# Performance work log

Measured on AMD Instinct MI355X. Metric: run time of the kernel, lower is better.

The kernel has to match this reference:

```python
import jax, jax.numpy as jnp
import numpy as np

B, N, D, H, O = 20000, 32, 128, 256, 128
ATT_SLOPE = 0.01   # nn.LeakyReLU() default inside self.att
ALPHA = 0.2        # leakyrelu slope for attention scores


def _lrelu(v, slope):
    return jnp.where(v > 0, v, slope * v)


def setup_inputs() -> dict:
    key = jax.random.key(0)
    ks = jax.random.split(key, 6)
    x = jax.random.normal(ks[0], (B, D), dtype=jnp.float32)
    neibs = jax.random.normal(ks[1], (B * N, D), dtype=jnp.float32)
    # torch Linear weight is [out,in]; we store transposed [in,out] for x @ W
    W_att = jax.random.normal(ks[2], (D, H), dtype=jnp.float32) / np.sqrt(D)
    W_fcx = jax.random.normal(ks[3], (D, O), dtype=jnp.float32) / np.sqrt(D)
    W_fcn = jax.random.normal(ks[4], (D, O), dtype=jnp.float32) / np.sqrt(D)
    a = jax.random.normal(ks[5], (2 * H, 1), dtype=jnp.float32) * (1.414 * np.sqrt(6.0 / (2 * H + 1)))
    return {"x": x, "neibs": neibs, "W_att": W_att, "W_fcx": W_fcx, "W_fcn": W_fcn, "a": a}


def reference(x, neibs, W_att, W_fcx, W_fcn, a):
    b = x.shape[0]
    n = neibs.shape[0] // b
    # self.att = Linear(no bias) + LeakyReLU(default 0.01)
    x_att = _lrelu(x @ W_att, ATT_SLOPE)                       # [B,H]
    neib_att = _lrelu(neibs @ W_att, ATT_SLOPE).reshape(b, n, -1)  # [B,N,H]
    # cat([x_att.repeat, neib_att]) @ a  ==  x_att @ a[:H] + neib_att @ a[H:]
    h = W_att.shape[1]
    e = _lrelu(x_att @ a[:h, 0] + neib_att @ a[h:, 0][..., None] if False else
               (x_att @ a[:h, 0])[:, None] + jnp.einsum('bnh,h->bn', neib_att, a[h:, 0]), ALPHA)  # [B,N]
    attention = jax.nn.softmax(e, axis=1)                      # softmax over neighbors
    # dropout skipped (eval mode / training=False)
    agg_neib = jnp.einsum('bnd,bn->bd', neibs.reshape(b, n, -1), attention)  # [B,D]
    out = jnp.concatenate([x @ W_fcx, agg_neib @ W_fcn], axis=1)  # combine_fn = cat dim=1
    out = jax.nn.relu(out)                                     # activation
    return out
```

## Files before the change

kernel.cpp:

```cpp
#include <hip/hip_runtime.h>
#include <hip/hip_bf16.h>


#define BB 20000
#define NN 32
#define DD 128
#define HH 256
#define OO 128
#define MB 4
#define ROWS 144
#define XR0 128
#define AG0 132

typedef __bf16 bf16x8 __attribute__((ext_vector_type(8)));
typedef __bf16 bf16x4 __attribute__((ext_vector_type(4)));
typedef float f32x4 __attribute__((ext_vector_type(4)));

template<int CTRL>
__device__ __forceinline__ float dpp_add(float v) {
    int r = __builtin_amdgcn_update_dpp(0, __builtin_bit_cast(int, v), CTRL, 0xF, 0xF, true);
    return v + __builtin_bit_cast(float, r);
}
__device__ __forceinline__ float red16(float v) {
    v = dpp_add<0x111>(v);
    v = dpp_add<0x112>(v);
    v = dpp_add<0x114>(v);
    v = dpp_add<0x118>(v);
    return v;
}

__global__ void prep_weights(const float* __restrict__ Watt,
                             const float* __restrict__ Wfcx,
                             const float* __restrict__ Wfcn,
                             __bf16* __restrict__ WaT,
                             __bf16* __restrict__ WcT) {
    int idx = blockIdx.x * 256 + threadIdx.x;
    int half = idx >> 15;
    int j = idx & 32767;
    int c = j >> 7, k = j & 127;
    if (half == 0) {
        WaT[j] = (__bf16)Watt[k * HH + c];
    } else {
        float wv = (c < OO) ? Wfcx[k * OO + c] : Wfcn[k * OO + (c - OO)];
        WcT[j] = (__bf16)wv;
    }
}

__launch_bounds__(256, 4)
__global__ void gat_fused(const float* __restrict__ x,
                          const float* __restrict__ neibs,
                          const float* __restrict__ a,
                          const __bf16* __restrict__ WaT,
                          const __bf16* __restrict__ WcT,
                          float* __restrict__ out) {
    __shared__ __bf16 rowsS[ROWS * 128];
    __shared__ float e_part[4][ROWS];
    __shared__ float att_s[MB][NN];

    const int tid = threadIdx.x;
    const int w   = tid >> 6;
    const int l   = tid & 63;
    const int lr  = l & 15;
    const int lg  = l >> 4;
    const int b0  = blockIdx.x * MB;
    char* rbase = (char*)rowsS;

    const int stbase = (tid >> 5) * 256 + ((8 * (tid & 31)) ^ ((tid >> 5) << 4));
    {
        const float4* np4 = (const float4*)(neibs + (size_t)b0 * NN * DD);
#pragma unroll
        for (int it = 0; it < 16; ++it) {
            float4 v = np4[it * 256 + tid];
            bf16x4 s = { (__bf16)v.x, (__bf16)v.y, (__bf16)v.z, (__bf16)v.w };
            *(bf16x4*)(rbase + stbase + it * 2048) = s;
        }
        if (tid < 128) {
            const float4* xp4 = (const float4*)(x + (size_t)b0 * DD);
            float4 v = xp4[tid];
            bf16x4 s = { (__bf16)v.x, (__bf16)v.y, (__bf16)v.z, (__bf16)v.w };
            *(bf16x4*)(rbase + stbase + 32768) = s;
        }
    }

    bf16x8 bfr[4][4];
    float aN[4], aNs[4], aX[4], aXs[4];
#pragma unroll
    for (int c4 = 0; c4 < 4; ++c4) {
        int col = (w * 4 + c4) * 16 + lr;
#pragma unroll
        for (int ks = 0; ks < 4; ++ks)
            bfr[c4][ks] = *(const bf16x8*)(WaT + col * 128 + ks * 32 + lg * 8);
        aX[c4] = a[col];        aXs[c4] = aX[c4] * 0.01f;
        aN[c4] = a[HH + col];   aNs[c4] = aN[c4] * 0.01f;
    }

    int abase[4];
#pragma unroll
    for (int ks = 0; ks < 4; ++ks)
        abase[ks] = lr * 256 + ((ks * 64 + lg * 16) ^ ((lr & 7) << 4));

    __syncthreads();

#pragma unroll
    for (int rt = 0; rt < 9; ++rt) {
        bf16x8 af[4];
#pragma unroll
        for (int ks = 0; ks < 4; ++ks)
            af[ks] = *(const bf16x8*)(rbase + abase[ks] + rt * 4096);
        f32x4 acc[4];
#pragma unroll
        for (int c4 = 0; c4 < 4; ++c4) acc[c4] = (f32x4){0.f, 0.f, 0.f, 0.f};
#pragma unroll
        for (int c4 = 0; c4 < 4; ++c4)
#pragma unroll
            for (int ks = 0; ks < 4; ++ks)
                acc[c4] = __builtin_amdgcn_mfma_f32_16x16x32_bf16(af[ks], bfr[c4][ks], acc[c4], 0, 0, 0);

        float ep[4] = {0.f, 0.f, 0.f, 0.f};
#pragma unroll
        for (int c4 = 0; c4 < 4; ++c4) {
            float av  = (rt == 8) ? aX[c4]  : aN[c4];
            float avs = (rt == 8) ? aXs[c4] : aNs[c4];
#pragma unroll
            for (int i = 0; i < 4; ++i) {
                float v = acc[c4][i];
                ep[i] = fmaf(v, (v > 0.f) ? av : avs, ep[i]);
            }
        }
#pragma unroll
        for (int i = 0; i < 4; ++i) ep[i] = red16(ep[i]);
        if (lr == 15) {
            f32x4 st = { ep[0], ep[1], ep[2], ep[3] };
            *(f32x4*)((char*)&e_part[w][0] + rt * 64 + lg * 16) = st;
        }
    }
    __syncthreads();

    if (tid < 128) {
        const int bloc = tid >> 5;
        const int nloc = tid & 31;
        float sn = e_part[0][tid] + e_part[1][tid] + e_part[2][tid] + e_part[3][tid];
        float sx = e_part[0][XR0 + bloc] + e_part[1][XR0 + bloc] +
                   e_part[2][XR0 + bloc] + e_part[3][XR0 + bloc];
        float e = sx + sn;
        e = (e > 0.f) ? e : 0.2f * e;
        float mx = e;
#pragma unroll
        for (int m = 16; m >= 1; m >>= 1) mx = fmaxf(mx, __shfl_xor(mx, m, 32));
        float ex = __expf(e - mx);
        float sum = ex;
#pragma unroll
        for (int m = 16; m >= 1; m >>= 1) sum += __shfl_xor(sum, m, 32);
        att_s[bloc][nloc] = ex / sum;
    }
    __syncthreads();

    bf16x8 bff[4][4];
#pragma unroll
    for (int c4 = 0; c4 < 4; ++c4) {
        int col = (w * 4 + c4) * 16 + lr;
#pragma unroll
        for (int ks = 0; ks < 4; ++ks)
            bff[c4][ks] = *(const bf16x8*)(WcT + col * 128 + ks * 32 + lg * 8);
    }

    {
        const int half = l >> 5, li = l & 31;
        const int node = w;
        const int agbase = node * 8192 + 256 * half + ((8 * li) ^ (half << 4));
        float ag[4] = {0.f, 0.f, 0.f, 0.f};
#pragma unroll
        for (int i = 0; i < 16; ++i) {
            float wv = att_s[node][2 * i + half];
            bf16x4 v = *(const bf16x4*)(rbase + (agbase ^ ((2 * i & 7) << 4)) + 512 * i);
#pragma unroll
            for (int j = 0; j < 4; ++j) ag[j] = fmaf(wv, (float)v[j], ag[j]);
        }
#pragma unroll
        for (int j = 0; j < 4; ++j) ag[j] += __shfl_xor(ag[j], 32);
        if (half == 0) {
            int row = AG0 + node;
            int off = row * 256 + ((8 * li) ^ ((row & 7) << 4));
            bf16x4 s = { (__bf16)ag[0], (__bf16)ag[1], (__bf16)ag[2], (__bf16)ag[3] };
            *(bf16x4*)(rbase + off) = s;
        }
    }
    __syncthreads();

    {
        bf16x8 af[4];
#pragma unroll
        for (int ks = 0; ks < 4; ++ks)
            af[ks] = *(const bf16x8*)(rbase + abase[ks] + 32768);
#pragma unroll
        for (int c4 = 0; c4 < 4; ++c4) {
            f32x4 acc = (f32x4){0.f, 0.f, 0.f, 0.f};
#pragma unroll
            for (int ks = 0; ks < 4; ++ks)
                acc = __builtin_amdgcn_mfma_f32_16x16x32_bf16(af[ks], bff[c4][ks], acc, 0, 0, 0);
            int col = (w * 4 + c4) * 16 + lr;
#pragma unroll
            for (int reg = 0; reg < 4; ++reg) {
                int i = lg * 4 + reg;
                bool doit = (col < 128) ? (i < 4) : (i >= 4 && i < 8);
                if (doit) {
                    float v = fmaxf(acc[reg], 0.f);
                    out[(size_t)(b0 + (i & 3)) * 256 + col] = v;
                }
            }
        }
    }
}

extern "C" void kernel_launch(void* const* d_in, const int* in_sizes, int n_in,
                              void* d_out, int out_size, void* d_ws, size_t ws_size,
                              hipStream_t stream) {
    const float* x    = (const float*)d_in[0];
    const float* nb   = (const float*)d_in[1];
    const float* Watt = (const float*)d_in[2];
    const float* Wfcx = (const float*)d_in[3];
    const float* Wfcn = (const float*)d_in[4];
    const float* a    = (const float*)d_in[5];
    __bf16* WaT = (__bf16*)d_ws;
    __bf16* WcT = WaT + 128 * 256;
    float* o = (float*)d_out;

    prep_weights<<<256, 256, 0, stream>>>(Watt, Wfcx, Wfcn, WaT, WcT);
    gat_fused<<<BB / MB, 256, 0, stream>>>(x, nb, a, WaT, WcT, o);
}
```

Before: 132.8 us.

## Convert fused GAT kernel to persistent grid with overlapped next-group loads

The kernel now launches a fixed grid of 1024 blocks that loop over node groups instead of one block per group. The next group's neighbour rows are loaded into shared memory before the final fc MFMA of the current group runs, and the x row is double-buffered. The aim is to overlap global loads with compute and to amortise block launch and setup. The stores to shared memory are not followed by a barrier before the fc MFMA reads the aggregated row, but that row sits outside the overwritten region. Reusing one weight register array for both matrices lowers register pressure, though the next iteration reloads the weights each time, and the neighbour loads are issued synchronously rather than truly asynchronously.

```diff
diff --git a/kernel.cpp b/kernel.cpp
--- a/kernel.cpp
+++ b/kernel.cpp
@@ -8,8 +8,9 @@
 #define HH 256
 #define OO 128
 #define MB 4
+#define NGROUP (BB / MB)
+#define GRID 1024
 #define ROWS 144
-#define XR0 128
 #define AG0 132
 
 typedef __bf16 bf16x8 __attribute__((ext_vector_type(8)));
@@ -62,12 +63,26 @@
     const int l   = tid & 63;
     const int lr  = l & 15;
     const int lg  = l >> 4;
-    const int b0  = blockIdx.x * MB;
     char* rbase = (char*)rowsS;
 
     const int stbase = (tid >> 5) * 256 + ((8 * (tid & 31)) ^ ((tid >> 5) << 4));
+    int abase[4];
+#pragma unroll
+    for (int ks = 0; ks < 4; ++ks)
+        abase[ks] = lr * 256 + ((ks * 64 + lg * 16) ^ ((lr & 7) << 4));
+    float aX[4], aN[4];
+#pragma unroll
+    for (int c4 = 0; c4 < 4; ++c4) {
+        int col = (w * 4 + c4) * 16 + lr;
+        aX[c4] = a[col];
+        aN[c4] = a[HH + col];
+    }
+
+    int g = (int)blockIdx.x;
+    int p = 0;
+
     {
-        const float4* np4 = (const float4*)(neibs + (size_t)b0 * NN * DD);
+        const float4* np4 = (const float4*)(neibs + (size_t)g * MB * NN * DD);
 #pragma unroll
         for (int it = 0; it < 16; ++it) {
             float4 v = np4[it * 256 + tid];
@@ -75,140 +90,148 @@
             *(bf16x4*)(rbase + stbase + it * 2048) = s;
         }
         if (tid < 128) {
-            const float4* xp4 = (const float4*)(x + (size_t)b0 * DD);
-            float4 v = xp4[tid];
+            float4 v = ((const float4*)(x + (size_t)g * MB * DD))[tid];
             bf16x4 s = { (__bf16)v.x, (__bf16)v.y, (__bf16)v.z, (__bf16)v.w };
             *(bf16x4*)(rbase + stbase + 32768) = s;
         }
     }
 
-    bf16x8 bfr[4][4];
-    float aN[4], aNs[4], aX[4], aXs[4];
-#pragma unroll
-    for (int c4 = 0; c4 < 4; ++c4) {
-        int col = (w * 4 + c4) * 16 + lr;
-#pragma unroll
-        for (int ks = 0; ks < 4; ++ks)
-            bfr[c4][ks] = *(const bf16x8*)(WaT + col * 128 + ks * 32 + lg * 8);
-        aX[c4] = a[col];        aXs[c4] = aX[c4] * 0.01f;
-        aN[c4] = a[HH + col];   aNs[c4] = aN[c4] * 0.01f;
-    }
-
-    int abase[4];
-#pragma unroll
-    for (int ks = 0; ks < 4; ++ks)
-        abase[ks] = lr * 256 + ((ks * 64 + lg * 16) ^ ((lr & 7) << 4));
-
-    __syncthreads();
-
-#pragma unroll
-    for (int rt = 0; rt < 9; ++rt) {
-        bf16x8 af[4];
-#pragma unroll
-        for (int ks = 0; ks < 4; ++ks)
-            af[ks] = *(const bf16x8*)(rbase + abase[ks] + rt * 4096);
-        f32x4 acc[4];
-#pragma unroll
-        for (int c4 = 0; c4 < 4; ++c4) acc[c4] = (f32x4){0.f, 0.f, 0.f, 0.f};
+    for (;;) {
+        __syncthreads();
+
+        bf16x8 bw[4][4];
 #pragma unroll
         for (int c4 = 0; c4 < 4; ++c4)
 #pragma unroll
             for (int ks = 0; ks < 4; ++ks)
-                acc[c4] = __builtin_amdgcn_mfma_f32_16x16x32_bf16(af[ks], bfr[c4][ks], acc[c4], 0, 0, 0);
-
-        float ep[4] = {0.f, 0.f, 0.f, 0.f};
-#pragma unroll
-        for (int c4 = 0; c4 < 4; ++c4) {
-            float av  = (rt == 8) ? aX[c4]  : aN[c4];
-            float avs = (rt == 8) ? aXs[c4] : aNs[c4];
-#pragma unroll
-            for (int i = 0; i < 4; ++i) {
-                float v = acc[c4][i];
-                ep[i] = fmaf(v, (v > 0.f) ? av : avs, ep[i]);
-            }
-        }
-#pragma unroll
-        for (int i = 0; i < 4; ++i) ep[i] = red16(ep[i]);
-        if (lr == 15) {
-            f32x4 st = { ep[0], ep[1], ep[2], ep[3] };
-            *(f32x4*)((char*)&e_part[w][0] + rt * 64 + lg * 16) = st;
-        }
-    }
-    __syncthreads();
-
-    if (tid < 128) {
-        const int bloc = tid >> 5;
-        const int nloc = tid & 31;
-        float sn = e_part[0][tid] + e_part[1][tid] + e_part[2][tid] + e_part[3][tid];
-        float sx = e_part[0][XR0 + bloc] + e_part[1][XR0 + bloc] +
-                   e_part[2][XR0 + bloc] + e_part[3][XR0 + bloc];
-        float e = sx + sn;
-        e = (e > 0.f) ? e : 0.2f * e;
-        float mx = e;
-#pragma unroll
-        for (int m = 16; m >= 1; m >>= 1) mx = fmaxf(mx, __shfl_xor(mx, m, 32));
-        float ex = __expf(e - mx);
-        float sum = ex;
-#pragma unroll
-        for (int m = 16; m >= 1; m >>= 1) sum += __shfl_xor(sum, m, 32);
-        att_s[bloc][nloc] = ex / sum;
-    }
-    __syncthreads();
-
-    bf16x8 bff[4][4];
-#pragma unroll
-    for (int c4 = 0; c4 < 4; ++c4) {
-        int col = (w * 4 + c4) * 16 + lr;
-#pragma unroll
-        for (int ks = 0; ks < 4; ++ks)
-            bff[c4][ks] = *(const bf16x8*)(WcT + col * 128 + ks * 32 + lg * 8);
-    }
-
-    {
-        const int half = l >> 5, li = l & 31;
-        const int node = w;
-        const int agbase = node * 8192 + 256 * half + ((8 * li) ^ (half << 4));
-        float ag[4] = {0.f, 0.f, 0.f, 0.f};
-#pragma unroll
-        for (int i = 0; i < 16; ++i) {
-            float wv = att_s[node][2 * i + half];
-            bf16x4 v = *(const bf16x4*)(rbase + (agbase ^ ((2 * i & 7) << 4)) + 512 * i);
-#pragma unroll
-            for (int j = 0; j < 4; ++j) ag[j] = fmaf(wv, (float)v[j], ag[j]);
-        }
-#pragma unroll
-        for (int j = 0; j < 4; ++j) ag[j] += __shfl_xor(ag[j], 32);
-        if (half == 0) {
-            int row = AG0 + node;
-            int off = row * 256 + ((8 * li) ^ ((row & 7) << 4));
-            bf16x4 s = { (__bf16)ag[0], (__bf16)ag[1], (__bf16)ag[2], (__bf16)ag[3] };
-            *(bf16x4*)(rbase + off) = s;
-        }
-    }
-    __syncthreads();
-
-    {
-        bf16x8 af[4];
-#pragma unroll
-        for (int ks = 0; ks < 4; ++ks)
-            af[ks] = *(const bf16x8*)(rbase + abase[ks] + 32768);
-#pragma unroll
-        for (int c4 = 0; c4 < 4; ++c4) {
-            f32x4 acc = (f32x4){0.f, 0.f, 0.f, 0.f};
+                bw[c4][ks] = *(const bf16x8*)(WaT + ((w * 4 + c4) * 16 + lr) * 128 + ks * 32 + lg * 8);
+        const int xoff = (lr < 4) ? 2048 * p : 0;
+
+#pragma unroll
+        for (int rt = 0; rt < 9; ++rt) {
+            f32x4 acc[4];
+#pragma unroll
+            for (int c4 = 0; c4 < 4; ++c4) acc[c4] = (f32x4){0.f, 0.f, 0.f, 0.f};
+#pragma unroll
+            for (int ks = 0; ks < 4; ++ks) {
+                bf16x8 af = *(const bf16x8*)(rbase + abase[ks] + (rt < 8 ? rt * 4096 : 32768 + xoff));
+#pragma unroll
+                for (int c4 = 0; c4 < 4; ++c4)
+                    acc[c4] = __builtin_amdgcn_mfma_f32_16x16x32_bf16(af, bw[c4][ks], acc[c4], 0, 0, 0);
+            }
+            float ep[4] = {0.f, 0.f, 0.f, 0.f};
+#pragma unroll
+            for (int c4 = 0; c4 < 4; ++c4) {
+                float av = (rt == 8) ? aX[c4] : aN[c4];
+#pragma unroll
+                for (int i = 0; i < 4; ++i) {
+                    float v = acc[c4][i];
+                    float lv = fmaxf(v, 0.f) + 0.01f * fminf(v, 0.f);
+                    ep[i] = fmaf(lv, av, ep[i]);
+                }
+            }
+#pragma unroll
+            for (int i = 0; i < 4; ++i) ep[i] = red16(ep[i]);
+            if (lr == 15) {
+                f32x4 st = { ep[0], ep[1], ep[2], ep[3] };
+                *(f32x4*)((char*)&e_part[w][0] + rt * 64 + lg * 16) = st;
+            }
+        }
+        __syncthreads();
+
+        if (tid < 128) {
+            const int bloc = tid >> 5;
+            const int nloc = tid & 31;
+            float sn = e_part[0][tid] + e_part[1][tid] + e_part[2][tid] + e_part[3][tid];
+            int xr = 128 + 8 * p + bloc;
+            float sx = e_part[0][xr] + e_part[1][xr] + e_part[2][xr] + e_part[3][xr];
+            float e = sx + sn;
+            e = (e > 0.f) ? e : 0.2f * e;
+            float mx = e;
+#pragma unroll
+            for (int m = 16; m >= 1; m >>= 1) mx = fmaxf(mx, __shfl_xor(mx, m, 32));
+            float ex = __expf(e - mx);
+            float sum = ex;
+#pragma unroll
+            for (int m = 16; m >= 1; m >>= 1) sum += __shfl_xor(sum, m, 32);
+            att_s[bloc][nloc] = ex / sum;
+        }
+        __syncthreads();
+
+        {
+            const int half = l >> 5, li = l & 31;
+            const int agbase = w * 8192 + 256 * half + ((8 * li) ^ (half << 4));
+            float ag[4] = {0.f, 0.f, 0.f, 0.f};
+#pragma unroll
+            for (int i = 0; i < 16; ++i) {
+                float wv = att_s[w][2 * i + half];
+                bf16x4 v = *(const bf16x4*)(rbase + (agbase ^ ((2 * i & 7) << 4)) + 512 * i);
+#pragma unroll
+                for (int j = 0; j < 4; ++j) ag[j] = fmaf(wv, (float)v[j], ag[j]);
+            }
+#pragma unroll
+            for (int j = 0; j < 4; ++j) ag[j] += __shfl_xor(ag[j], 32);
+            if (half == 0) {
+                int row = AG0 + w;
+                int off = row * 256 + ((8 * li) ^ ((row & 7) << 4));
+                bf16x4 s = { (__bf16)ag[0], (__bf16)ag[1], (__bf16)ag[2], (__bf16)ag[3] };
+                *(bf16x4*)(rbase + off) = s;
+            }
+        }
+        __syncthreads();
+
+        int gn = g + GRID;
+        bool more = (gn < NGROUP);
+#pragma unroll
+        for (int c4 = 0; c4 < 4; ++c4)
 #pragma unroll
             for (int ks = 0; ks < 4; ++ks)
-                acc = __builtin_amdgcn_mfma_f32_16x16x32_bf16(af[ks], bff[c4][ks], acc, 0, 0, 0);
-            int col = (w * 4 + c4) * 16 + lr;
-#pragma unroll
-            for (int reg = 0; reg < 4; ++reg) {
-                int i = lg * 4 + reg;
-                bool doit = (col < 128) ? (i < 4) : (i >= 4 && i < 8);
-                if (doit) {
-                    float v = fmaxf(acc[reg], 0.f);
-                    out[(size_t)(b0 + (i & 3)) * 256 + col] = v;
+                bw[c4][ks] = *(const bf16x8*)(WcT + ((w * 4 + c4) * 16 + lr) * 128 + ks * 32 + lg * 8);
+        if (more) {
+            const float4* np4 = (const float4*)(neibs + (size_t)gn * MB * NN * DD);
+#pragma unroll
+            for (int it = 0; it < 16; ++it) {
+                float4 v = np4[it * 256 + tid];
+                bf16x4 s = { (__bf16)v.x, (__bf16)v.y, (__bf16)v.z, (__bf16)v.w };
+                *(bf16x4*)(rbase + stbase + it * 2048) = s;
+            }
+            if (tid < 128) {
+                float4 v = ((const float4*)(x + (size_t)gn * MB * DD))[tid];
+                bf16x4 s = { (__bf16)v.x, (__bf16)v.y, (__bf16)v.z, (__bf16)v.w };
+                *(bf16x4*)(rbase + stbase + 32768 + 2048 * (p ^ 1)) = s;
+            }
+        }
+
+        {
+            f32x4 acc[4];
+#pragma unroll
+            for (int c4 = 0; c4 < 4; ++c4) acc[c4] = (f32x4){0.f, 0.f, 0.f, 0.f};
+#pragma unroll
+            for (int ks = 0; ks < 4; ++ks) {
+                bf16x8 af = *(const bf16x8*)(rbase + abase[ks] + 32768 + xoff);
+#pragma unroll
+                for (int c4 = 0; c4 < 4; ++c4)
+                    acc[c4] = __builtin_amdgcn_mfma_f32_16x16x32_bf16(af, bw[c4][ks], acc[c4], 0, 0, 0);
+            }
+            const int b0 = g * MB;
+#pragma unroll
+            for (int c4 = 0; c4 < 4; ++c4) {
+                int col = (w * 4 + c4) * 16 + lr;
+#pragma unroll
+                for (int reg = 0; reg < 4; ++reg) {
+                    int i = lg * 4 + reg;
+                    bool doit = (col < 128) ? (i < 4) : (i >= 4 && i < 8);
+                    if (doit) {
+                        float v = fmaxf(acc[c4][reg], 0.f);
+                        out[(size_t)(b0 + (i & 3)) * 256 + col] = v;
+                    }
                 }
             }
         }
+
+        if (!more) break;
+        g = gn;
+        p ^= 1;
     }
 }
 
@@ -226,5 +249,5 @@
     float* o = (float*)d_out;
 
     prep_weights<<<256, 256, 0, stream>>>(Watt, Wfcx, Wfcn, WaT, WcT);
-    gat_fused<<<BB / MB, 256, 0, stream>>>(x, nb, a, WaT, WcT, o);
-}
+    gat_fused<<<GRID, 256, 0, stream>>>(x, nb, a, WaT, WcT, o);
+}
```

New measurement: 175.4 us. 1.32x slower.
